# Kernel optimization log

Hardware: AMD Instinct MI355X
Metric: run time of the kernel (lower is better)

## Reference

```python
import jax, jax.numpy as jnp
import numpy as np

K = 20          # neighbors
BN_EPS = 1e-5


def _knn_idx(x, k):
    """x: [B, C, N] -> idx of k nearest neighbors [B, N, k] (by squared distance, self included)."""
    xx = jnp.sum(x * x, axis=1)                       # [B, N]
    inner = jnp.einsum('bcn,bcm->bnm', x, x)          # [B, N, N]
    neg_sqdist = 2.0 * inner - xx[:, :, None] - xx[:, None, :]
    return jax.lax.top_k(neg_sqdist, k)[1]            # [B, N, k]


def _graph_feature(x, k):
    """x: [B, C, N] -> edge features cat(x_j - x_i, x_i): [B, 2C, N, k]."""
    idx = _knn_idx(x, k)                              # [B, N, k]
    xT = x.transpose(0, 2, 1)                         # [B, N, C]
    nbrs = jax.vmap(lambda xt, ii: xt[ii])(xT, idx)   # [B, N, k, C] gather
    center = xT[:, :, None, :]                        # [B, N, 1, C]
    feat = jnp.concatenate(
        [nbrs - center, jnp.broadcast_to(center, nbrs.shape)], axis=-1)  # [B, N, k, 2C]
    return feat.transpose(0, 3, 1, 2)                 # [B, 2C, N, k]


def _conv_bn_lrelu(feat, W, gamma, beta, mean, var):
    """1x1 Conv2d (no bias) + BatchNorm (given stats) + LeakyReLU(0.2). feat: [B, Cin, N, k]."""
    y = jnp.einsum('oc,bcnk->bonk', W, feat)
    scale = (gamma / jnp.sqrt(var + BN_EPS))[None, :, None, None]
    y = (y - mean[None, :, None, None]) * scale + beta[None, :, None, None]
    return jnp.where(y > 0, y, 0.2 * y)


def setup_inputs() -> dict:
    key = jax.random.key(0)
    ks = list(jax.random.split(key, 32))
    B, N = 8, 1024
    f32 = jnp.float32

    def w(kk, o, i):
        return jax.random.normal(kk, (o, i), dtype=f32) / np.sqrt(i)

    def bn(k1, k2, k3, k4, c):
        g = jax.random.uniform(k1, (c,), dtype=f32, minval=0.5, maxval=1.5)
        b = jax.random.normal(k2, (c,), dtype=f32) * 0.05
        m = jax.random.normal(k3, (c,), dtype=f32) * 0.05
        v = jax.random.uniform(k4, (c,), dtype=f32, minval=0.5, maxval=1.5)
        return g, b, m, v

    x = jax.random.normal(ks[0], (B, N, 3), dtype=f32)
    W0 = w(ks[1], 64, 6);    g0, b0, m0, v0 = bn(ks[2], ks[3], ks[4], ks[5], 64)
    W1 = w(ks[6], 128, 128); g1, b1, m1, v1 = bn(ks[7], ks[8], ks[9], ks[10], 128)
    W2 = w(ks[11], 256, 256); g2, b2, m2, v2 = bn(ks[12], ks[13], ks[14], ks[15], 256)
    Wf = w(ks[16], 512, 896); gf, bf, mf, vf = bn(ks[17], ks[18], ks[19], ks[20], 512)
    We = w(ks[21], 256, 512)
    return dict(x=x,
                W0=W0, g0=g0, b0=b0, m0=m0, v0=v0,
                W1=W1, g1=g1, b1=b1, m1=m1, v1=v1,
                W2=W2, g2=g2, b2=b2, m2=m2, v2=v2,
                Wf=Wf, gf=gf, bf=bf, mf=mf, vf=vf,
                We=We)


def reference(x, W0, g0, b0, m0, v0, W1, g1, b1, m1, v1,
              W2, g2, b2, m2, v2, Wf, gf, bf, mf, vf, We):
    h = x.transpose(0, 2, 1)                          # [B, 3, N]
    outs = []
    for (W, g, b, m, v) in ((W0, g0, b0, m0, v0),
                            (W1, g1, b1, m1, v1),
                            (W2, g2, b2, m2, v2)):
        gfeat = _graph_feature(h, K)                  # [B, 2C, N, k]
        y = _conv_bn_lrelu(gfeat, W, g, b, m, v)      # [B, Cout, N, k]
        h = y.mean(axis=-1)                           # max-free EdgeConv pool over k
        outs.append(h)
    cat = jnp.concatenate(outs, axis=1)               # [B, 448, N]
    gfeat = _graph_feature(cat, K)                    # [B, 896, N, k]
    y = _conv_bn_lrelu(gfeat, Wf, gf, bf, mf, vf)     # [B, 512, N, k]
    pooled = y.mean(axis=-1).mean(axis=-1)            # [B, 512] (pool over k then N)
    return pooled @ We.T                              # [B, num_features]
```

## Files before the change

### kernel.cpp

```cpp
#include <hip/hip_runtime.h>
#include <cstdint>

#define KNN 20
#define BV 8
#define NV 1024

template <int CTRL>
__device__ __forceinline__ unsigned dppmax(unsigned x) {
    unsigned m = (unsigned)__builtin_amdgcn_update_dpp((int)x, (int)x, CTRL, 0xf, 0xf, false);
    return (x > m) ? x : m;
}
template <int CTRL>
__device__ __forceinline__ unsigned dppmin(unsigned x) {
    unsigned m = (unsigned)__builtin_amdgcn_update_dpp((int)x, (int)x, CTRL, 0xf, 0xf, false);
    return (x < m) ? x : m;
}
__device__ __forceinline__ unsigned wave_max_u32(unsigned x) {
    x = dppmax<0xB1>(x); x = dppmax<0x4E>(x); x = dppmax<0x141>(x);
    x = dppmax<0x140>(x); x = dppmax<0x142>(x); x = dppmax<0x143>(x);
    return (unsigned)__builtin_amdgcn_readlane((int)x, 63);
}
__device__ __forceinline__ unsigned wave_min_u32(unsigned x) {
    x = dppmin<0xB1>(x); x = dppmin<0x4E>(x); x = dppmin<0x141>(x);
    x = dppmin<0x140>(x); x = dppmin<0x142>(x); x = dppmin<0x143>(x);
    return (unsigned)__builtin_amdgcn_readlane((int)x, 63);
}

__global__ __launch_bounds__(256) void k_transpose(const float* __restrict__ x, float* __restrict__ hx) {
    int id = blockIdx.x * 256 + threadIdx.x;
    if (id >= BV * 3 * NV) return;
    int n = id % NV;
    int c = (id / NV) % 3;
    int b = id / (3 * NV);
    hx[id] = x[(b * NV + n) * 3 + c];
}

__global__ __launch_bounds__(256) void k_xx(const float* __restrict__ h, float* __restrict__ xx,
                                            int C, int bstride) {
    int id = blockIdx.x * 256 + threadIdx.x;
    int n = id % NV, b = id / NV;
    if (b >= BV) return;
    const float* hp = h + (size_t)b * bstride + n;
    float s = 0.f;
    for (int c = 0; c < C; ++c) { float v = hp[(size_t)c * NV]; s += v * v; }
    xx[b * NV + n] = s;
}

__global__ __launch_bounds__(512, 4) void k_knn(const float* __restrict__ h, const float* __restrict__ xx,
                                                int C, int bstride,
                                                unsigned* __restrict__ sval, int* __restrict__ sidx) {
    __shared__ float Bs[8][512];
    __shared__ float As[8][32];
    const int tile = blockIdx.x, half = blockIdx.y, b = blockIdx.z;
    const int i0 = tile * 32, jbase = half * 512;
    const int t = threadIdx.x, lane = t & 63, w = t >> 6;
    const int irow = i0 + w * 4;
    float acc[4][8] = {};
    const float* hb = h + (size_t)b * bstride;

    for (int c0 = 0; c0 < C; c0 += 8) {
        __syncthreads();
#pragma unroll
        for (int r = 0; r < 2; ++r) {
            int e = r * 512 + t;
            int cc = e >> 7, g = e & 127;
            float4 v = make_float4(0.f, 0.f, 0.f, 0.f);
            if (c0 + cc < C) v = *(const float4*)&hb[(size_t)(c0 + cc) * NV + jbase + g * 4];
            *(float4*)&Bs[cc][g * 4] = v;
        }
        if (t < 64) {
#pragma unroll
            for (int r = 0; r < 4; ++r) {
                int e = r * 64 + t;
                int cc = e >> 5, ii = e & 31;
                As[cc][ii] = (c0 + cc < C) ? hb[(size_t)(c0 + cc) * NV + i0 + ii] : 0.f;
            }
        }
        __syncthreads();
#pragma unroll
        for (int c = 0; c < 8; ++c) {
            float4 arv = *(const float4*)&As[c][w * 4];
            float ar[4] = {arv.x, arv.y, arv.z, arv.w};
            float4 b0 = *(const float4*)&Bs[c][lane * 8];
            float4 b1 = *(const float4*)&Bs[c][lane * 8 + 4];
            float br[8] = {b0.x, b0.y, b0.z, b0.w, b1.x, b1.y, b1.z, b1.w};
#pragma unroll
            for (int a = 0; a < 4; ++a)
#pragma unroll
                for (int q = 0; q < 8; ++q) acc[a][q] += ar[a] * br[q];
        }
    }

    const float* xb = xx + b * NV;
    float4 x0 = *(const float4*)&xb[jbase + lane * 8];
    float4 x1 = *(const float4*)&xb[jbase + lane * 8 + 4];
    float xxj[8] = {x0.x, x0.y, x0.z, x0.w, x1.x, x1.y, x1.z, x1.w};
#pragma unroll
    for (int a = 0; a < 4; ++a) {
        float xi = xb[irow + a];
#pragma unroll
        for (int q = 0; q < 8; ++q) acc[a][q] = 2.f * acc[a][q] - xi - xxj[q];
    }

#pragma unroll 1
    for (int s = 0; s < KNN; ++s) {
#pragma unroll
        for (int a = 0; a < 4; ++a) {
            float v0[4]; int q0[4];
#pragma unroll
            for (int i = 0; i < 4; ++i) {
                bool g = acc[a][2 * i + 1] > acc[a][2 * i];
                v0[i] = g ? acc[a][2 * i + 1] : acc[a][2 * i];
                q0[i] = g ? 2 * i + 1 : 2 * i;
            }
            float v1[2]; int q1[2];
#pragma unroll
            for (int i = 0; i < 2; ++i) {
                bool g = v0[2 * i + 1] > v0[2 * i];
                v1[i] = g ? v0[2 * i + 1] : v0[2 * i];
                q1[i] = g ? q0[2 * i + 1] : q0[2 * i];
            }
            bool gf = v1[1] > v1[0];
            float bv = gf ? v1[1] : v1[0];
            int bq = gf ? q1[1] : q1[0];

            unsigned u = __float_as_uint(bv);
            unsigned su = ((int)u < 0) ? ~u : (u | 0x80000000u);
            int myj = jbase + lane * 8 + bq;
            unsigned gmax = wave_max_u32(su);
            unsigned cand = (su == gmax) ? (unsigned)myj : 0xFFFFFFFFu;
            int j = (int)wave_min_u32(cand);
            if (lane == 0) {
                size_t o = ((size_t)(b * NV + irow + a) * 2 + half) * KNN + s;
                sval[o] = gmax;
                sidx[o] = j;
            }
            int wq = (myj == j && su == gmax) ? bq : 99;
#pragma unroll
            for (int q = 0; q < 8; ++q)
                if (wq == q) acc[a][q] = -3.4e38f;
        }
    }
}

__global__ __launch_bounds__(256) void k_merge(const unsigned* __restrict__ sval,
                                               const int* __restrict__ sidx,
                                               int* __restrict__ idx) {
    int row = blockIdx.x * 256 + threadIdx.x;
    if (row >= BV * NV) return;
    const unsigned* v0 = sval + (size_t)row * 2 * KNN;
    const unsigned* v1 = v0 + KNN;
    const int* i0p = sidx + (size_t)row * 2 * KNN;
    const int* i1p = i0p + KNN;
    int* op = idx + (size_t)row * KNN;
    int a = 0, c = 0;
#pragma unroll
    for (int s = 0; s < KNN; ++s) {
        unsigned va = v0[a], vb = v1[c];
        int ia = i0p[a], ib = i1p[c];
        bool take0 = (va > vb) || (va == vb && ia < ib);
        op[s] = take0 ? ia : ib;
        a += take0 ? 1 : 0;
        c += take0 ? 0 : 1;
    }
}

__global__ __launch_bounds__(256) void k_pack(const float* __restrict__ W, float* __restrict__ wb,
                                              int C, int O) {
    int id = blockIdx.x * 256 + threadIdx.x;
    if (id >= 2 * O * C) return;
    int c = id % C, o = (id / C) % O, half = id / (C * O);
    float wl = W[(size_t)o * 2 * C + c];
    wb[id] = half ? (W[(size_t)o * 2 * C + C + c] - wl) : wl;
}

__global__ __launch_bounds__(256) void k_gemm(const float* __restrict__ A, int astride,
                                              const float* __restrict__ h, int bstride, int C,
                                              float* __restrict__ out, int O) {
    __shared__ float Ws[8][64], Hs[8][128];
    const int b = blockIdx.z, o0 = blockIdx.y * 64, n0 = blockIdx.x * 128;
    const int t = threadIdx.x, tx = t & 15, ty = t >> 4;
    float acc[4][8] = {};
    const float* hb = h + (size_t)b * bstride;
    for (int c0 = 0; c0 < C; c0 += 8) {
#pragma unroll
        for (int q = 0; q < 2; ++q) {
            int e = t + q * 256;
            int oo = e >> 3, cc = e & 7;
            Ws[cc][oo] = ((c0 + cc) < C) ? A[(size_t)(o0 + oo) * astride + c0 + cc] : 0.f;
        }
        {
            int cc = t >> 5, nn4 = t & 31;
            float4 v = make_float4(0.f, 0.f, 0.f, 0.f);
            if (c0 + cc < C) v = *(const float4*)&hb[(size_t)(c0 + cc) * NV + n0 + nn4 * 4];
            *(float4*)&Hs[cc][nn4 * 4] = v;
        }
        __syncthreads();
#pragma unroll
        for (int c = 0; c < 8; ++c) {
            float4 wv = *(const float4*)&Ws[c][ty * 4];
            float ar[4] = {wv.x, wv.y, wv.z, wv.w};
            float br[8];
            float4 h0 = *(const float4*)&Hs[c][tx * 4];
            float4 h1 = *(const float4*)&Hs[c][64 + tx * 4];
            br[0] = h0.x; br[1] = h0.y; br[2] = h0.z; br[3] = h0.w;
            br[4] = h1.x; br[5] = h1.y; br[6] = h1.z; br[7] = h1.w;
#pragma unroll
            for (int a = 0; a < 4; ++a)
#pragma unroll
                for (int q = 0; q < 8; ++q) acc[a][q] += ar[a] * br[q];
        }
        __syncthreads();
    }
#pragma unroll
    for (int a = 0; a < 4; ++a) {
        int o = o0 + ty * 4 + a;
        float* outp = out + ((size_t)b * O + o) * NV + n0;
        float4 s0 = make_float4(acc[a][0], acc[a][1], acc[a][2], acc[a][3]);
        float4 s1 = make_float4(acc[a][4], acc[a][5], acc[a][6], acc[a][7]);
        *(float4*)&outp[tx * 4] = s0;
        *(float4*)&outp[64 + tx * 4] = s1;
    }
}

__global__ __launch_bounds__(256) void k_edge(const float* __restrict__ pd,
                                              const int* __restrict__ idx,
                                              const float* __restrict__ ga, const float* __restrict__ be,
                                              const float* __restrict__ mu, const float* __restrict__ va,
                                              float* __restrict__ out, int out_bstride, int O) {
    const int n = blockIdx.x * 256 + threadIdx.x;
    const int o = blockIdx.y, b = blockIdx.z;
    const float a  = ga[o] / sqrtf(va[o] + 1e-5f);
    const float c0 = be[o] - mu[o] * a;
    const float* pb = pd + ((size_t)b * 2 * O + o) * NV;
    const float dv  = pd[((size_t)b * 2 * O + O + o) * NV + n];
    const int* ip   = idx + ((size_t)b * NV + n) * KNN;
    float s = 0.f;
#pragma unroll
    for (int k = 0; k < KNN; ++k) {
        int j = ip[k];
        float y = fmaf(a, pb[j] + dv, c0);
        s += (y > 0.f) ? y : 0.2f * y;
    }
    out[(size_t)b * out_bstride + (size_t)o * NV + n] = s * (1.f / KNN);
}

__global__ __launch_bounds__(256) void k_pool(const float* __restrict__ hf, float* __restrict__ pooled) {
    const int o = blockIdx.x, b = blockIdx.y;
    const float* hp = hf + ((size_t)b * 512 + o) * NV;
    float s = 0.f;
    for (int i = threadIdx.x; i < NV; i += 256) s += hp[i];
#pragma unroll
    for (int off = 32; off > 0; off >>= 1) s += __shfl_down(s, off, 64);
    __shared__ float red[4];
    if ((threadIdx.x & 63) == 0) red[threadIdx.x >> 6] = s;
    __syncthreads();
    if (threadIdx.x == 0)
        pooled[(size_t)b * 512 + o] = (red[0] + red[1] + red[2] + red[3]) * (1.f / NV);
}

__global__ __launch_bounds__(256) void k_final(const float* __restrict__ pooled, const float* __restrict__ We,
                                               float* __restrict__ out) {
    const int j = threadIdx.x, b = blockIdx.x;
    __shared__ float ps[512];
    for (int o = threadIdx.x; o < 512; o += 256) ps[o] = pooled[b * 512 + o];
    __syncthreads();
    float s = 0.f;
    for (int o = 0; o < 512; ++o) s += ps[o] * We[(size_t)j * 512 + o];
    out[b * 256 + j] = s;
}

extern "C" void kernel_launch(void* const* d_in, const int* in_sizes, int n_in,
                              void* d_out, int out_size, void* d_ws, size_t ws_size,
                              hipStream_t stream) {
    const float* x  = (const float*)d_in[0];
    const float* W0 = (const float*)d_in[1];
    const float* g0 = (const float*)d_in[2];
    const float* b0 = (const float*)d_in[3];
    const float* m0 = (const float*)d_in[4];
    const float* v0 = (const float*)d_in[5];
    const float* W1 = (const float*)d_in[6];
    const float* g1 = (const float*)d_in[7];
    const float* b1 = (const float*)d_in[8];
    const float* m1 = (const float*)d_in[9];
    const float* v1 = (const float*)d_in[10];
    const float* W2 = (const float*)d_in[11];
    const float* g2 = (const float*)d_in[12];
    const float* b2 = (const float*)d_in[13];
    const float* m2 = (const float*)d_in[14];
    const float* v2 = (const float*)d_in[15];
    const float* Wf = (const float*)d_in[16];
    const float* gf = (const float*)d_in[17];
    const float* bf = (const float*)d_in[18];
    const float* mf = (const float*)d_in[19];
    const float* vf = (const float*)d_in[20];
    const float* We = (const float*)d_in[21];

    float* ws = (float*)d_ws;
    float* hx     = ws;
    float* cat    = hx + 24576;
    float* xx     = cat + 3670016;
    int*   idx    = (int*)(xx + 8192);
    float* pd     = (float*)(idx + 163840);
    float* wb     = pd + 8388608;
    float* hf     = wb + 458752;
    float* pooled = hf + 4194304;
    unsigned* sval = (unsigned*)(pooled + 4096);
    int*      sidx = (int*)(sval + 327680);

    k_transpose<<<96, 256, 0, stream>>>(x, hx);

    auto run_layer = [&](const float* h, int C, int bstride, const float* W,
                         const float* g, const float* be, const float* m, const float* v,
                         int O, float* outp, int obstride) {
        k_xx<<<32, 256, 0, stream>>>(h, xx, C, bstride);
        k_knn<<<dim3(32, 2, 8), 512, 0, stream>>>(h, xx, C, bstride, sval, sidx);
        k_merge<<<32, 256, 0, stream>>>(sval, sidx, idx);
        int pn = 2 * O * C;
        k_pack<<<(pn + 255) / 256, 256, 0, stream>>>(W, wb, C, O);
        k_gemm<<<dim3(8, 2 * O / 64, 8), 256, 0, stream>>>(wb, C, h, bstride, C, pd, 2 * O);
        k_edge<<<dim3(4, O, 8), 256, 0, stream>>>(pd, idx, g, be, m, v, outp, obstride, O);
    };

    run_layer(hx, 3, 3 * NV, W0, g0, b0, m0, v0, 64, cat, 448 * NV);
    run_layer(cat, 64, 448 * NV, W1, g1, b1, m1, v1, 128, cat + 64 * NV, 448 * NV);
    run_layer(cat + 64 * NV, 128, 448 * NV, W2, g2, b2, m2, v2, 256, cat + 192 * NV, 448 * NV);
    run_layer(cat, 448, 448 * NV, Wf, gf, bf, mf, vf, 512, hf, 512 * NV);

    k_pool<<<dim3(512, 8), 256, 0, stream>>>(hf, pooled);
    k_final<<<8, 256, 0, stream>>>(pooled, We, (float*)d_out);
}
```

Baseline: 890.0 us.

## Split kNN into quarter panels, 4-way merge, and batch-major grid ordering

```diff
diff --git a/kernel.cpp b/kernel.cpp
--- a/kernel.cpp
+++ b/kernel.cpp
@@ -46,24 +46,24 @@
     xx[b * NV + n] = s;
 }
 
-__global__ __launch_bounds__(512, 4) void k_knn(const float* __restrict__ h, const float* __restrict__ xx,
+__global__ __launch_bounds__(512, 8) void k_knn(const float* __restrict__ h, const float* __restrict__ xx,
                                                 int C, int bstride,
                                                 unsigned* __restrict__ sval, int* __restrict__ sidx) {
-    __shared__ float Bs[8][512];
+    __shared__ float Bs[8][256];
     __shared__ float As[8][32];
-    const int tile = blockIdx.x, half = blockIdx.y, b = blockIdx.z;
-    const int i0 = tile * 32, jbase = half * 512;
+    const int bx = blockIdx.x;
+    const int tile = bx >> 5, panel = bx & 31;
+    const int b = panel & 7, quarter = panel >> 3;
+    const int i0 = tile * 32, jbase = quarter * 256;
     const int t = threadIdx.x, lane = t & 63, w = t >> 6;
     const int irow = i0 + w * 4;
-    float acc[4][8] = {};
+    float acc[4][4] = {};
     const float* hb = h + (size_t)b * bstride;
 
     for (int c0 = 0; c0 < C; c0 += 8) {
         __syncthreads();
-#pragma unroll
-        for (int r = 0; r < 2; ++r) {
-            int e = r * 512 + t;
-            int cc = e >> 7, g = e & 127;
+        {
+            int cc = t >> 6, g = t & 63;
             float4 v = make_float4(0.f, 0.f, 0.f, 0.f);
             if (c0 + cc < C) v = *(const float4*)&hb[(size_t)(c0 + cc) * NV + jbase + g * 4];
             *(float4*)&Bs[cc][g * 4] = v;
@@ -81,63 +81,51 @@
         for (int c = 0; c < 8; ++c) {
             float4 arv = *(const float4*)&As[c][w * 4];
             float ar[4] = {arv.x, arv.y, arv.z, arv.w};
-            float4 b0 = *(const float4*)&Bs[c][lane * 8];
-            float4 b1 = *(const float4*)&Bs[c][lane * 8 + 4];
-            float br[8] = {b0.x, b0.y, b0.z, b0.w, b1.x, b1.y, b1.z, b1.w};
+            float4 bv = *(const float4*)&Bs[c][lane * 4];
+            float br[4] = {bv.x, bv.y, bv.z, bv.w};
 #pragma unroll
             for (int a = 0; a < 4; ++a)
 #pragma unroll
-                for (int q = 0; q < 8; ++q) acc[a][q] += ar[a] * br[q];
+                for (int q = 0; q < 4; ++q) acc[a][q] += ar[a] * br[q];
         }
     }
 
     const float* xb = xx + b * NV;
-    float4 x0 = *(const float4*)&xb[jbase + lane * 8];
-    float4 x1 = *(const float4*)&xb[jbase + lane * 8 + 4];
-    float xxj[8] = {x0.x, x0.y, x0.z, x0.w, x1.x, x1.y, x1.z, x1.w};
+    float4 xv = *(const float4*)&xb[jbase + lane * 4];
+    float xxj[4] = {xv.x, xv.y, xv.z, xv.w};
 #pragma unroll
     for (int a = 0; a < 4; ++a) {
         float xi = xb[irow + a];
 #pragma unroll
-        for (int q = 0; q < 8; ++q) acc[a][q] = 2.f * acc[a][q] - xi - xxj[q];
+        for (int q = 0; q < 4; ++q) acc[a][q] = 2.f * acc[a][q] - xi - xxj[q];
     }
 
 #pragma unroll 1
     for (int s = 0; s < KNN; ++s) {
 #pragma unroll
         for (int a = 0; a < 4; ++a) {
-            float v0[4]; int q0[4];
-#pragma unroll
-            for (int i = 0; i < 4; ++i) {
-                bool g = acc[a][2 * i + 1] > acc[a][2 * i];
-                v0[i] = g ? acc[a][2 * i + 1] : acc[a][2 * i];
-                q0[i] = g ? 2 * i + 1 : 2 * i;
-            }
-            float v1[2]; int q1[2];
-#pragma unroll
-            for (int i = 0; i < 2; ++i) {
-                bool g = v0[2 * i + 1] > v0[2 * i];
-                v1[i] = g ? v0[2 * i + 1] : v0[2 * i];
-                q1[i] = g ? q0[2 * i + 1] : q0[2 * i];
-            }
-            bool gf = v1[1] > v1[0];
-            float bv = gf ? v1[1] : v1[0];
-            int bq = gf ? q1[1] : q1[0];
+            bool g0 = acc[a][1] > acc[a][0];
+            float v0 = g0 ? acc[a][1] : acc[a][0]; int q0 = g0 ? 1 : 0;
+            bool g1 = acc[a][3] > acc[a][2];
+            float v1 = g1 ? acc[a][3] : acc[a][2]; int q1 = g1 ? 3 : 2;
+            bool gf = v1 > v0;
+            float bv = gf ? v1 : v0;
+            int bq = gf ? q1 : q0;
 
             unsigned u = __float_as_uint(bv);
             unsigned su = ((int)u < 0) ? ~u : (u | 0x80000000u);
-            int myj = jbase + lane * 8 + bq;
+            int myj = jbase + (lane << 2) + bq;
             unsigned gmax = wave_max_u32(su);
             unsigned cand = (su == gmax) ? (unsigned)myj : 0xFFFFFFFFu;
             int j = (int)wave_min_u32(cand);
             if (lane == 0) {
-                size_t o = ((size_t)(b * NV + irow + a) * 2 + half) * KNN + s;
+                size_t o = ((size_t)(b * NV + irow + a) * 4 + quarter) * KNN + s;
                 sval[o] = gmax;
                 sidx[o] = j;
             }
-            int wq = (myj == j && su == gmax) ? bq : 99;
-#pragma unroll
-            for (int q = 0; q < 8; ++q)
+            int wq = (myj == j) ? bq : 9;
+#pragma unroll
+            for (int q = 0; q < 4; ++q)
                 if (wq == q) acc[a][q] = -3.4e38f;
         }
     }
@@ -148,20 +136,31 @@
                                                int* __restrict__ idx) {
     int row = blockIdx.x * 256 + threadIdx.x;
     if (row >= BV * NV) return;
-    const unsigned* v0 = sval + (size_t)row * 2 * KNN;
-    const unsigned* v1 = v0 + KNN;
-    const int* i0p = sidx + (size_t)row * 2 * KNN;
-    const int* i1p = i0p + KNN;
+    const unsigned* v = sval + (size_t)row * 4 * KNN;
+    const int* ii = sidx + (size_t)row * 4 * KNN;
+    int pos[4] = {0, 0, 0, 0};
+    unsigned hv[4]; int hj[4];
+#pragma unroll
+    for (int l = 0; l < 4; ++l) { hv[l] = v[l * KNN]; hj[l] = ii[l * KNN]; }
     int* op = idx + (size_t)row * KNN;
-    int a = 0, c = 0;
-#pragma unroll
+#pragma unroll 1
     for (int s = 0; s < KNN; ++s) {
-        unsigned va = v0[a], vb = v1[c];
-        int ia = i0p[a], ib = i1p[c];
-        bool take0 = (va > vb) || (va == vb && ia < ib);
-        op[s] = take0 ? ia : ib;
-        a += take0 ? 1 : 0;
-        c += take0 ? 0 : 1;
+        bool b01 = (hv[1] > hv[0]) || (hv[1] == hv[0] && hj[1] < hj[0]);
+        unsigned v01 = b01 ? hv[1] : hv[0]; int j01 = b01 ? hj[1] : hj[0]; int l01 = b01 ? 1 : 0;
+        bool b23 = (hv[3] > hv[2]) || (hv[3] == hv[2] && hj[3] < hj[2]);
+        unsigned v23 = b23 ? hv[3] : hv[2]; int j23 = b23 ? hj[3] : hj[2]; int l23 = b23 ? 3 : 2;
+        bool bf = (v23 > v01) || (v23 == v01 && j23 < j01);
+        int win = bf ? l23 : l01;
+        op[s] = bf ? j23 : j01;
+#pragma unroll
+        for (int l = 0; l < 4; ++l) {
+            if (win == l) {
+                int np = pos[l] + 1; pos[l] = np;
+                bool ok = np < KNN;
+                hv[l] = ok ? v[l * KNN + np] : 0u;
+                hj[l] = ok ? ii[l * KNN + np] : 0x7FFFFFFF;
+            }
+        }
     }
 }
 
@@ -178,7 +177,7 @@
                                               const float* __restrict__ h, int bstride, int C,
                                               float* __restrict__ out, int O) {
     __shared__ float Ws[8][64], Hs[8][128];
-    const int b = blockIdx.z, o0 = blockIdx.y * 64, n0 = blockIdx.x * 128;
+    const int b = blockIdx.x, n0 = blockIdx.y * 128, o0 = blockIdx.z * 64;
     const int t = threadIdx.x, tx = t & 15, ty = t >> 4;
     float acc[4][8] = {};
     const float* hb = h + (size_t)b * bstride;
@@ -228,21 +227,28 @@
                                               const float* __restrict__ ga, const float* __restrict__ be,
                                               const float* __restrict__ mu, const float* __restrict__ va,
                                               float* __restrict__ out, int out_bstride, int O) {
-    const int n = blockIdx.x * 256 + threadIdx.x;
-    const int o = blockIdx.y, b = blockIdx.z;
-    const float a  = ga[o] / sqrtf(va[o] + 1e-5f);
-    const float c0 = be[o] - mu[o] * a;
-    const float* pb = pd + ((size_t)b * 2 * O + o) * NV;
-    const float dv  = pd[((size_t)b * 2 * O + O + o) * NV + n];
-    const int* ip   = idx + ((size_t)b * NV + n) * KNN;
-    float s = 0.f;
-#pragma unroll
-    for (int k = 0; k < KNN; ++k) {
-        int j = ip[k];
-        float y = fmaf(a, pb[j] + dv, c0);
-        s += (y > 0.f) ? y : 0.2f * y;
-    }
-    out[(size_t)b * out_bstride + (size_t)o * NV + n] = s * (1.f / KNN);
+    const int b = blockIdx.x;
+    const int n = blockIdx.y * 256 + threadIdx.x;
+    const int o0 = blockIdx.z * 4;
+    const int* ip = idx + ((size_t)b * NV + n) * KNN;
+    int jj[KNN];
+#pragma unroll
+    for (int k = 0; k < KNN; ++k) jj[k] = ip[k];
+#pragma unroll
+    for (int a = 0; a < 4; ++a) {
+        const int o = o0 + a;
+        const float al = ga[o] / sqrtf(va[o] + 1e-5f);
+        const float c0 = be[o] - mu[o] * al;
+        const float* pb = pd + ((size_t)b * 2 * O + o) * NV;
+        const float dv  = pd[((size_t)b * 2 * O + O + o) * NV + n];
+        float s = 0.f;
+#pragma unroll
+        for (int k = 0; k < KNN; ++k) {
+            float y = fmaf(al, pb[jj[k]] + dv, c0);
+            s += (y > 0.f) ? y : 0.2f * y;
+        }
+        out[(size_t)b * out_bstride + (size_t)o * NV + n] = s * (1.f / KNN);
+    }
 }
 
 __global__ __launch_bounds__(256) void k_pool(const float* __restrict__ hf, float* __restrict__ pooled) {
@@ -306,7 +312,7 @@
     float* hf     = wb + 458752;
     float* pooled = hf + 4194304;
     unsigned* sval = (unsigned*)(pooled + 4096);
-    int*      sidx = (int*)(sval + 327680);
+    int*      sidx = (int*)(sval + 655360);
 
     k_transpose<<<96, 256, 0, stream>>>(x, hx);
 
@@ -314,12 +320,12 @@
                          const float* g, const float* be, const float* m, const float* v,
                          int O, float* outp, int obstride) {
         k_xx<<<32, 256, 0, stream>>>(h, xx, C, bstride);
-        k_knn<<<dim3(32, 2, 8), 512, 0, stream>>>(h, xx, C, bstride, sval, sidx);
+        k_knn<<<1024, 512, 0, stream>>>(h, xx, C, bstride, sval, sidx);
         k_merge<<<32, 256, 0, stream>>>(sval, sidx, idx);
         int pn = 2 * O * C;
         k_pack<<<(pn + 255) / 256, 256, 0, stream>>>(W, wb, C, O);
-        k_gemm<<<dim3(8, 2 * O / 64, 8), 256, 0, stream>>>(wb, C, h, bstride, C, pd, 2 * O);
-        k_edge<<<dim3(4, O, 8), 256, 0, stream>>>(pd, idx, g, be, m, v, outp, obstride, O);
+        k_gemm<<<dim3(8, 8, 2 * O / 64), 256, 0, stream>>>(wb, C, h, bstride, C, pd, 2 * O);
+        k_edge<<<dim3(8, 4, O / 4), 256, 0, stream>>>(pd, idx, g, be, m, v, outp, obstride, O);
     };
 
     run_layer(hx, 3, 3 * NV, W0, g0, b0, m0, v0, 64, cat, 448 * NV);
```

Result: slower. 935.4 us (+5.1%).
